# Performance work log

Measured on AMD Instinct MI355X. Metric: run time of the kernel, lower is better.

The kernel has to match this reference:

```python
import jax, jax.numpy as jnp
import numpy as np

T = 256        # number of save/step points
BATCH = 2048   # batched trajectories
DATA = 32      # state dim (data_size)
WIDTH = 128    # MLP width
DELAYS = (1.0, 2.0)  # constant delays tau_j (all >> dt so lookups are in the past)


def setup_inputs() -> dict:
    key = jax.random.key(0)
    ks = jax.random.split(key, 5)
    ts = jnp.linspace(0.0, 10.0, T, dtype=jnp.float32)
    y0 = jax.random.normal(ks[0], (BATCH, DATA), dtype=jnp.float32)
    in_size = (len(DELAYS) + 1) * DATA  # (nb_delays + 1) * data_size

    def lin(k, o, i):
        kw, kb = jax.random.split(k)
        lim = 1.0 / np.sqrt(i)
        W = jax.random.uniform(kw, (o, i), jnp.float32, -lim, lim)
        b = jax.random.uniform(kb, (o,), jnp.float32, -lim, lim)
        return W, b

    W0, b0 = lin(ks[1], WIDTH, in_size)   # in -> width
    W1, b1 = lin(ks[2], WIDTH, WIDTH)     # hidden
    W2, b2 = lin(ks[3], WIDTH, WIDTH)     # hidden
    W3, b3 = lin(ks[4], DATA, WIDTH)      # width -> out (no activation)
    return dict(ts=ts, y0=y0, W0=W0, b0=b0, W1=W1, b1=b1, W2=W2, b2=b2, W3=W3, b3=b3)


def _mlp(x, W0, b0, W1, b1, W2, b2, W3, b3):
    # eqx.nn.MLP(depth=3, activation=relu): 4 linears, relu after hidden layers
    h = jax.nn.relu(x @ W0.T + b0)
    h = jax.nn.relu(h @ W1.T + b1)
    h = jax.nn.relu(h @ W2.T + b2)
    return h @ W3.T + b3


def _solve(ts, y0, params):
    t0 = ts[0]
    dt0 = ts[1] - ts[0]

    def lookup(buf, t):
        # linear interpolation of stored history on the uniform grid;
        # t <= t0 clips to index 0 where buf[0] == y0 (constant initial history)
        s = jnp.clip((t - t0) / dt0, 0.0, T - 1.0)
        i0 = jnp.floor(s).astype(jnp.int32)
        i1 = jnp.minimum(i0 + 1, T - 1)
        w = s - i0.astype(s.dtype)
        return (1.0 - w) * buf[i0] + w * buf[i1]

    def f(t, y, buf):
        hist = [lookup(buf, t - tau) for tau in DELAYS]
        return _mlp(jnp.concatenate([y] + hist, axis=-1), *params)

    buf0 = jnp.zeros((T, BATCH, DATA), y0.dtype).at[0].set(y0)

    def step(carry, inp):
        y, buf = carry
        i, t, t_next = inp
        dt = t_next - t
        # Bosh3 / Bogacki-Shampine stages
        k1 = f(t, y, buf)
        k2 = f(t + 0.5 * dt, y + 0.5 * dt * k1, buf)
        k3 = f(t + 0.75 * dt, y + 0.75 * dt * k2, buf)
        y_next = y + dt * (2.0 / 9.0 * k1 + 1.0 / 3.0 * k2 + 4.0 / 9.0 * k3)
        buf = buf.at[i + 1].set(y_next)
        return (y_next, buf), y_next

    xs = (jnp.arange(T - 1), ts[:-1], ts[1:])
    (_, _), ys_tail = jax.lax.scan(step, (y0, buf0), xs)
    return jnp.concatenate([y0[None], ys_tail], axis=0)  # [T, BATCH, DATA]


def reference(ts, y0, W0, b0, W1, b1, W2, b2, W3, b3):
    ys = _solve(ts, y0, (W0, b0, W1, b1, W2, b2, W3, b3))
    return ys, jnp.int32(T - 1)  # (solution.ys, num_steps)
```

## Files before the change

### kernel.cpp

```cpp
#include <hip/hip_runtime.h>

#define TT 256
#define BATCH 2048
#define DATA 32
#define WSLOTS 52

typedef __bf16 bf16x8 __attribute__((ext_vector_type(8)));
typedef float f32x4 __attribute__((ext_vector_type(4)));

#define MFMA(A, B, C) __builtin_amdgcn_mfma_f32_16x16x32_bf16((A), (B), (C), 0, 0, 0)

union bfp2 { uint2 u; __bf16 b[4]; };
union bfp4 { uint4 q; bf16x8 v; __bf16 b[8]; };

__device__ __forceinline__ bf16x8 ldw8(const float* __restrict__ p) {
    float4 a = *(const float4*)p;
    float4 b = *(const float4*)(p + 4);
    bf16x8 r;
    r[0] = (__bf16)a.x; r[1] = (__bf16)a.y; r[2] = (__bf16)a.z; r[3] = (__bf16)a.w;
    r[4] = (__bf16)b.x; r[5] = (__bf16)b.y; r[6] = (__bf16)b.z; r[7] = (__bf16)b.w;
    return r;
}

__device__ __forceinline__ bf16x8 ldx(const char* base, int row, int kbyte) {
    return *(const bf16x8*)(base + row * 256 + (kbyte ^ ((row & 7) << 4)));
}

#define LERP2(TQT, O1, O2)                                                            \
    {                                                                                 \
        _Pragma("unroll") for (int dl = 0; dl < 2; ++dl) {                            \
            const float tau = dl ? 2.0f : 1.0f;                                       \
            float s = ((TQT) - tau - t0v) * ivd0;                                     \
            s = fminf(fmaxf(s, 0.0f), 255.0f);                                        \
            const int   i0 = (int)s;                                                  \
            const int   i1 = min(i0 + 1, TT - 1);                                     \
            const float w  = s - (float)i0;                                           \
            bfp4 pa, pb, pr;                                                          \
            pa.v = *(const bf16x8*)(hists + (i0 % WSLOTS) * 1280 + m * 80 + g * 16);  \
            pb.v = *(const bf16x8*)(hists + (i1 % WSLOTS) * 1280 + m * 80 + g * 16);  \
            _Pragma("unroll") for (int e = 0; e < 8; ++e) {                           \
                const float va = (float)pa.b[e];                                      \
                pr.b[e] = (__bf16)fmaf(w, (float)pb.b[e] - va, va);                   \
            }                                                                         \
            if (dl == 0) O1 = pr.v; else O2 = pr.v;                                   \
        }                                                                             \
    }

#define SEGB()                                                                        \
    {                                                                                 \
        bf16x8 xf[4];                                                                 \
        _Pragma("unroll") for (int kc = 0; kc < 4; ++kc)                              \
            xf[kc] = ldx(hA, m, kc * 64 + g * 16);                                    \
        f32x4 a0 = b1D, cc = {0.f, 0.f, 0.f, 0.f};                                    \
        __builtin_amdgcn_s_setprio(1);                                                \
        a0 = MFMA(W1f[0], xf[0], a0); cc = MFMA(W1f[2], xf[2], cc);                   \
        a0 = MFMA(W1f[1], xf[1], a0); cc = MFMA(W1f[3], xf[3], cc);                   \
        __builtin_amdgcn_s_setprio(0);                                                \
        bfp2 p0;                                                                      \
        _Pragma("unroll") for (int j = 0; j < 4; ++j)                                 \
            p0.b[j] = (__bf16)fmaxf(a0[j] + cc[j], 0.0f);                             \
        *(uint2*)(hB + m * 256 + ((tbB2 + g * 8) ^ sw)) = p0.u;                       \
    }

#define SEGC(COEF, FIRST, STOREH2, DSTBUF)                                            \
    {                                                                                 \
        bf16x8 xf[4];                                                                 \
        _Pragma("unroll") for (int kc = 0; kc < 4; ++kc)                              \
            xf[kc] = ldx(hB, m, kc * 64 + g * 16);                                    \
        f32x4 a0 = b2D, cc = {0.f, 0.f, 0.f, 0.f};                                    \
        __builtin_amdgcn_s_setprio(1);                                                \
        a0 = MFMA(W2f[0], xf[0], a0); cc = MFMA(W2f[2], xf[2], cc);                   \
        a0 = MFMA(W2f[1], xf[1], a0); cc = MFMA(W2f[3], xf[3], cc);                   \
        __builtin_amdgcn_s_setprio(0);                                                \
        f32x4 r;                                                                      \
        _Pragma("unroll") for (int j = 0; j < 4; ++j)                                 \
            r[j] = fmaxf(a0[j] + cc[j], 0.0f);                                        \
        if (FIRST) { _Pragma("unroll") for (int j = 0; j < 4; ++j)                    \
                         hsreg[j] = (COEF) * r[j]; }                                  \
        else       { _Pragma("unroll") for (int j = 0; j < 4; ++j)                    \
                         hsreg[j] = fmaf((COEF), r[j], hsreg[j]); }                   \
        bfp2 ph;                                                                      \
        if (STOREH2) { _Pragma("unroll") for (int j = 0; j < 4; ++j)                  \
                           ph.b[j] = (__bf16)r[j]; }                                  \
        else         { _Pragma("unroll") for (int j = 0; j < 4; ++j)                  \
                           ph.b[j] = (__bf16)hsreg[j]; }                              \
        *(uint2*)((DSTBUF) + m * 256 + ((tbB2 + g * 8) ^ sw)) = ph.u;                 \
    }

#define SEGA23(HIN, CST)                                                              \
    {                                                                                 \
        bf16x8 hf[4];                                                                 \
        _Pragma("unroll") for (int kc = 0; kc < 4; ++kc)                              \
            hf[kc] = ldx(HIN, m, kc * 64 + g * 16);                                   \
        f32x4 ta = {0.f, 0.f, 0.f, 0.f}, tc = ta;                                     \
        __builtin_amdgcn_s_setprio(1);                                                \
        ta = MFMA(Mf[0], hf[0], ta); tc = MFMA(Mf[2], hf[2], tc);                     \
        ta = MFMA(Mf[1], hf[1], ta); tc = MFMA(Mf[3], hf[3], tc);                     \
        __builtin_amdgcn_s_setprio(0);                                                \
        bf16x8 xl1, xl2;                                                              \
        LERP2(fmaf(CST, dt, t), xl1, xl2)                                             \
        f32x4 la = b0D;                                                               \
        __builtin_amdgcn_s_setprio(1);                                                \
        la = MFMA(W0lf[0], xl1, la);                                                  \
        la = MFMA(W0lf[1], xl2, la);                                                  \
        __builtin_amdgcn_s_setprio(0);                                                \
        const float cdt = (CST) * dt;                                                 \
        bfp2 p0;                                                                      \
        _Pragma("unroll") for (int j = 0; j < 4; ++j)                                 \
            p0.b[j] = (__bf16)fmaxf(fmaf(cdt, ta[j] + tc[j] + c0v[j], u[j]) + la[j],  \
                                    0.0f);                                            \
        *(uint2*)(hA + m * 256 + ((tbB2 + g * 8) ^ sw)) = p0.u;                       \
    }

__global__ __launch_bounds__(512, 1) void dde_fu(
    const float* __restrict__ ts, const float* __restrict__ y0,
    const float* __restrict__ W0, const float* __restrict__ b0,
    const float* __restrict__ W1, const float* __restrict__ b1,
    const float* __restrict__ W2, const float* __restrict__ b2,
    const float* __restrict__ W3, const float* __restrict__ b3,
    float* __restrict__ out)
{
    __shared__ __align__(16) char hists[WSLOTS * 1280];
    __shared__ __align__(16) char hA[16 * 256];
    __shared__ __align__(16) char hB[16 * 256];
    __shared__ __align__(16) char h2a[16 * 256];
    __shared__ __align__(16) char h2b[16 * 256];
    __shared__ __align__(16) char hsb[16 * 256];
    __shared__ __align__(16) float ybuf[512];
    __shared__ float tsb[TT];

    const int tid  = threadIdx.x;
    const int lane = tid & 63;
    const int wv   = tid >> 6;
    const int m    = lane & 15;
    const int g    = lane >> 4;
    const int tbB2 = wv * 32;
    const int sw   = (m & 7) << 4;
    const int R0   = blockIdx.x * 16;

    for (int idx = tid; idx < WSLOTS * 320; idx += 512) ((unsigned*)hists)[idx] = 0u;
    if (tid < TT) tsb[tid] = ts[tid];

    bf16x8 W0lf[2], W1f[4], W2f[4], W3f[4], Mf[4];
    {
        const int rw = wv * 16 + m;
        #pragma unroll
        for (int kc = 0; kc < 2; ++kc) W0lf[kc] = ldw8(W0 + rw * 96 + 32 + kc * 32 + g * 8);
        #pragma unroll
        for (int kc = 0; kc < 4; ++kc) W1f[kc] = ldw8(W1 + rw * 128 + kc * 32 + g * 8);
        #pragma unroll
        for (int kc = 0; kc < 4; ++kc) W2f[kc] = ldw8(W2 + rw * 128 + kc * 32 + g * 8);
        const int rw3 = (wv & 1) * 16 + m;
        #pragma unroll
        for (int kc = 0; kc < 4; ++kc) W3f[kc] = ldw8(W3 + rw3 * 128 + kc * 32 + g * 8);
    }
    {
        float w0y[32];
        const float* w0r = W0 + (wv * 16 + m) * 96;
        #pragma unroll
        for (int d = 0; d < 32; ++d) w0y[d] = w0r[d];
        #pragma unroll
        for (int kc = 0; kc < 4; ++kc) {
            bf16x8 f;
            #pragma unroll
            for (int e = 0; e < 8; ++e) {
                const int h = kc * 32 + g * 8 + e;
                float acc = 0.f;
                #pragma unroll
                for (int d = 0; d < 32; ++d) acc = fmaf(w0y[d], W3[d * 128 + h], acc);
                f[e] = (__bf16)acc;
            }
            Mf[kc] = f;
        }
    }
    f32x4 b0D = *(const f32x4*)(b0 + wv * 16 + g * 4);
    f32x4 b1D = *(const f32x4*)(b1 + wv * 16 + g * 4);
    f32x4 b2D = *(const f32x4*)(b2 + wv * 16 + g * 4);
    f32x4 b3D = *(const f32x4*)(b3 + (wv & 1) * 16 + g * 4);
    f32x4 c0v, u;
    {
        const float* yr = y0 + (R0 + m) * DATA;
        #pragma unroll
        for (int j = 0; j < 4; ++j) {
            const float* w0r = W0 + (wv * 16 + g * 4 + j) * 96;
            float a = 0.f, uu = 0.f;
            #pragma unroll
            for (int d = 0; d < 32; ++d) {
                a  = fmaf(w0r[d], b3[d], a);
                uu = fmaf(w0r[d], yr[d], uu);
            }
            c0v[j] = a; u[j] = uu;
        }
    }
    f32x4 y;
    #pragma unroll
    for (int j = 0; j < 4; ++j)
        y[j] = y0[(R0 + m) * DATA + (wv & 1) * 16 + g * 4 + j];

    __syncthreads();

    if (wv == 0) {
        float4 v0 = *(const float4*)(y0 + (R0 + m) * DATA + g * 8);
        float4 v1 = *(const float4*)(y0 + (R0 + m) * DATA + g * 8 + 4);
        bfp4 p;
        p.b[0] = (__bf16)v0.x; p.b[1] = (__bf16)v0.y;
        p.b[2] = (__bf16)v0.z; p.b[3] = (__bf16)v0.w;
        p.b[4] = (__bf16)v1.x; p.b[5] = (__bf16)v1.y;
        p.b[6] = (__bf16)v1.z; p.b[7] = (__bf16)v1.w;
        *(bf16x8*)(hists + m * 80 + g * 16) = p.v;
        *(float4*)(out + (R0 + m) * DATA + g * 8) = v0;
        *(float4*)(out + (R0 + m) * DATA + g * 8 + 4) = v1;
    }
    if (blockIdx.x == 0 && tid == 0)
        out[(size_t)TT * BATCH * DATA] = 255.0f;
    __syncthreads();

    const float t0v  = tsb[0];
    const float ivd0 = 1.0f / (tsb[1] - tsb[0]);

    #pragma unroll 1
    for (int i = 0; i < TT - 1; ++i) {
        const float t  = tsb[i];
        const float dt = tsb[i + 1] - t;
        f32x4 hsreg;

        {
            if (i > 0) {
                const float dtp = t - tsb[i - 1];
                bf16x8 hs[4];
                #pragma unroll
                for (int kc = 0; kc < 4; ++kc) hs[kc] = ldx(hsb, m, kc * 64 + g * 16);
                f32x4 ta = {0.f, 0.f, 0.f, 0.f}, tc = ta;
                __builtin_amdgcn_s_setprio(1);
                ta = MFMA(Mf[0], hs[0], ta); tc = MFMA(Mf[2], hs[2], tc);
                ta = MFMA(Mf[1], hs[1], ta); tc = MFMA(Mf[3], hs[3], tc);
                __builtin_amdgcn_s_setprio(0);
                #pragma unroll
                for (int j = 0; j < 4; ++j)
                    u[j] = fmaf(dtp, ta[j] + tc[j] + c0v[j], u[j]);
                if (wv < 2) {
                    f32x4 ya = {0.f, 0.f, 0.f, 0.f}, yc = ya;
                    __builtin_amdgcn_s_setprio(1);
                    ya = MFMA(W3f[0], hs[0], ya); yc = MFMA(W3f[2], hs[2], yc);
                    ya = MFMA(W3f[1], hs[1], ya); yc = MFMA(W3f[3], hs[3], yc);
                    __builtin_amdgcn_s_setprio(0);
                    #pragma unroll
                    for (int j = 0; j < 4; ++j) {
                        y[j] = fmaf(dtp, ya[j] + yc[j] + b3D[j], y[j]);
                        *(__bf16*)(hists + (i % WSLOTS) * 1280 + m * 80
                                   + wv * 32 + g * 8 + 2 * j) = (__bf16)y[j];
                        ybuf[m * 32 + wv * 16 + g * 4 + j] = y[j];
                    }
                }
            }
            bf16x8 xl1, xl2;
            LERP2(t, xl1, xl2)
            f32x4 la = b0D;
            __builtin_amdgcn_s_setprio(1);
            la = MFMA(W0lf[0], xl1, la);
            la = MFMA(W0lf[1], xl2, la);
            __builtin_amdgcn_s_setprio(0);
            bfp2 p0;
            #pragma unroll
            for (int j = 0; j < 4; ++j)
                p0.b[j] = (__bf16)fmaxf(u[j] + la[j], 0.0f);
            *(uint2*)(hA + m * 256 + ((tbB2 + g * 8) ^ sw)) = p0.u;
        }
        __syncthreads();
        SEGB()
        __syncthreads();
        SEGC(2.0f / 9.0f, 1, 1, h2a)
        if (i > 0 && wv < 2) {
            const int L = wv * 64 + lane;
            float4 yv = *(const float4*)(ybuf + L * 4);
            *(float4*)(out + (size_t)i * BATCH * DATA
                       + (R0 + (L >> 3)) * DATA + (L & 7) * 4) = yv;
        }
        __syncthreads();
        SEGA23(h2a, 0.5f)
        __syncthreads();
        SEGB()
        __syncthreads();
        SEGC(1.0f / 3.0f, 0, 1, h2b)
        __syncthreads();
        SEGA23(h2b, 0.75f)
        __syncthreads();
        SEGB()
        __syncthreads();
        SEGC(4.0f / 9.0f, 0, 0, hsb)
        __syncthreads();
    }

    if (wv < 2) {
        const float dtp = tsb[TT - 1] - tsb[TT - 2];
        bf16x8 hs[4];
        #pragma unroll
        for (int kc = 0; kc < 4; ++kc) hs[kc] = ldx(hsb, m, kc * 64 + g * 16);
        f32x4 ya = {0.f, 0.f, 0.f, 0.f}, yc = ya;
        ya = MFMA(W3f[0], hs[0], ya); yc = MFMA(W3f[2], hs[2], yc);
        ya = MFMA(W3f[1], hs[1], ya); yc = MFMA(W3f[3], hs[3], yc);
        #pragma unroll
        for (int j = 0; j < 4; ++j) {
            y[j] = fmaf(dtp, ya[j] + yc[j] + b3D[j], y[j]);
            ybuf[m * 32 + (wv & 1) * 16 + g * 4 + j] = y[j];
        }
    }
    __syncthreads();
    if (wv < 2) {
        const int L = wv * 64 + lane;
        float4 yv = *(const float4*)(ybuf + L * 4);
        *(float4*)(out + (size_t)(TT - 1) * BATCH * DATA
                   + (R0 + (L >> 3)) * DATA + (L & 7) * 4) = yv;
    }
}

extern "C" void kernel_launch(void* const* d_in, const int* in_sizes, int n_in,
                              void* d_out, int out_size, void* d_ws, size_t ws_size,
                              hipStream_t stream) {
    const float* ts = (const float*)d_in[0];
    const float* y0 = (const float*)d_in[1];
    const float* W0 = (const float*)d_in[2];
    const float* b0 = (const float*)d_in[3];
    const float* W1 = (const float*)d_in[4];
    const float* b1 = (const float*)d_in[5];
    const float* W2 = (const float*)d_in[6];
    const float* b2 = (const float*)d_in[7];
    const float* W3 = (const float*)d_in[8];
    const float* b3 = (const float*)d_in[9];

    dde_fu<<<dim3(BATCH / 16), dim3(512), 0, stream>>>(
        ts, y0, W0, b0, W1, b1, W2, b2, W3, b3, (float*)d_out);
}
```

Baseline: 842.0 us.

## Prefetch delayed-history interpolation into the previous stage and build the fused matrix with MFMA

```diff
diff --git a/kernel.cpp b/kernel.cpp
--- a/kernel.cpp
+++ b/kernel.cpp
@@ -46,7 +46,7 @@
         }                                                                             \
     }
 
-#define SEGB()                                                                        \
+#define SEGB_PF(TQ2, O1, O2)                                                          \
     {                                                                                 \
         bf16x8 xf[4];                                                                 \
         _Pragma("unroll") for (int kc = 0; kc < 4; ++kc)                              \
@@ -56,6 +56,7 @@
         a0 = MFMA(W1f[0], xf[0], a0); cc = MFMA(W1f[2], xf[2], cc);                   \
         a0 = MFMA(W1f[1], xf[1], a0); cc = MFMA(W1f[3], xf[3], cc);                   \
         __builtin_amdgcn_s_setprio(0);                                                \
+        LERP2(TQ2, O1, O2)                                                            \
         bfp2 p0;                                                                      \
         _Pragma("unroll") for (int j = 0; j < 4; ++j)                                 \
             p0.b[j] = (__bf16)fmaxf(a0[j] + cc[j], 0.0f);                             \
@@ -87,22 +88,18 @@
         *(uint2*)((DSTBUF) + m * 256 + ((tbB2 + g * 8) ^ sw)) = ph.u;                 \
     }
 
-#define SEGA23(HIN, CST)                                                              \
+#define SEGA_F(HIN, CST, XL1, XL2)                                                    \
     {                                                                                 \
         bf16x8 hf[4];                                                                 \
         _Pragma("unroll") for (int kc = 0; kc < 4; ++kc)                              \
             hf[kc] = ldx(HIN, m, kc * 64 + g * 16);                                   \
+        f32x4 la = b0D;                                                               \
         f32x4 ta = {0.f, 0.f, 0.f, 0.f}, tc = ta;                                     \
         __builtin_amdgcn_s_setprio(1);                                                \
+        la = MFMA(W0lf[0], XL1, la);                 \
+        la = MFMA(W0lf[1], XL2, la);                                                  \
         ta = MFMA(Mf[0], hf[0], ta); tc = MFMA(Mf[2], hf[2], tc);                     \
         ta = MFMA(Mf[1], hf[1], ta); tc = MFMA(Mf[3], hf[3], tc);                     \
-        __builtin_amdgcn_s_setprio(0);                                                \
-        bf16x8 xl1, xl2;                                                              \
-        LERP2(fmaf(CST, dt, t), xl1, xl2)                                             \
-        f32x4 la = b0D;                                                               \
-        __builtin_amdgcn_s_setprio(1);                                                \
-        la = MFMA(W0lf[0], xl1, la);                                                  \
-        la = MFMA(W0lf[1], xl2, la);                                                  \
         __builtin_amdgcn_s_setprio(0);                                                \
         const float cdt = (CST) * dt;                                                 \
         bfp2 p0;                                                                      \
@@ -112,7 +109,7 @@
         *(uint2*)(hA + m * 256 + ((tbB2 + g * 8) ^ sw)) = p0.u;                       \
     }
 
-__global__ __launch_bounds__(512, 1) void dde_fu(
+__global__ __launch_bounds__(512, 1) void dde_f2(
     const float* __restrict__ ts, const float* __restrict__ y0,
     const float* __restrict__ W0, const float* __restrict__ b0,
     const float* __restrict__ W1, const float* __restrict__ b1,
@@ -121,6 +118,7 @@
     float* __restrict__ out)
 {
     __shared__ __align__(16) char hists[WSLOTS * 1280];
+    __shared__ __align__(16) char Mlds[128 * 256];
     __shared__ __align__(16) char hA[16 * 256];
     __shared__ __align__(16) char hB[16 * 256];
     __shared__ __align__(16) char h2a[16 * 256];
@@ -141,7 +139,7 @@
     for (int idx = tid; idx < WSLOTS * 320; idx += 512) ((unsigned*)hists)[idx] = 0u;
     if (tid < TT) tsb[tid] = ts[tid];
 
-    bf16x8 W0lf[2], W1f[4], W2f[4], W3f[4], Mf[4];
+    bf16x8 W0lf[2], W1f[4], W2f[4], W3f[4];
     {
         const int rw = wv * 16 + m;
         #pragma unroll
@@ -155,22 +153,21 @@
         for (int kc = 0; kc < 4; ++kc) W3f[kc] = ldw8(W3 + rw3 * 128 + kc * 32 + g * 8);
     }
     {
-        float w0y[32];
-        const float* w0r = W0 + (wv * 16 + m) * 96;
-        #pragma unroll
-        for (int d = 0; d < 32; ++d) w0y[d] = w0r[d];
-        #pragma unroll
-        for (int kc = 0; kc < 4; ++kc) {
-            bf16x8 f;
+        bf16x8 Af = ldw8(W0 + (wv * 16 + m) * 96 + g * 8);
+        #pragma unroll
+        for (int ht = 0; ht < 8; ++ht) {
+            bf16x8 Bf;
             #pragma unroll
-            for (int e = 0; e < 8; ++e) {
-                const int h = kc * 32 + g * 8 + e;
-                float acc = 0.f;
-                #pragma unroll
-                for (int d = 0; d < 32; ++d) acc = fmaf(w0y[d], W3[d * 128 + h], acc);
-                f[e] = (__bf16)acc;
+            for (int e = 0; e < 8; ++e)
+                Bf[e] = (__bf16)W3[(g * 8 + e) * 128 + ht * 16 + m];
+            f32x4 d = {0.f, 0.f, 0.f, 0.f};
+            d = MFMA(Af, Bf, d);
+            #pragma unroll
+            for (int j = 0; j < 4; ++j) {
+                const int r = wv * 16 + g * 4 + j;
+                *(__bf16*)(Mlds + r * 256 + (((ht * 16 + m) * 2) ^ ((r & 7) << 4)))
+                    = (__bf16)d[j];
             }
-            Mf[kc] = f;
         }
     }
     f32x4 b0D = *(const f32x4*)(b0 + wv * 16 + g * 4);
@@ -198,6 +195,10 @@
         y[j] = y0[(R0 + m) * DATA + (wv & 1) * 16 + g * 4 + j];
 
     __syncthreads();
+
+    bf16x8 Mf[4];
+    #pragma unroll
+    for (int kc = 0; kc < 4; ++kc) Mf[kc] = ldx(Mlds, wv * 16 + m, kc * 64 + g * 16);
 
     if (wv == 0) {
         float4 v0 = *(const float4*)(y0 + (R0 + m) * DATA + g * 8);
@@ -218,10 +219,14 @@
     const float t0v  = tsb[0];
     const float ivd0 = 1.0f / (tsb[1] - tsb[0]);
 
+    bf16x8 xl1a, xl1b, xl2a, xl2b, xl3a, xl3b;
+    LERP2(t0v, xl1a, xl1b)
+
     #pragma unroll 1
     for (int i = 0; i < TT - 1; ++i) {
         const float t  = tsb[i];
-        const float dt = tsb[i + 1] - t;
+        const float tn = tsb[i + 1];
+        const float dt = tn - t;
         f32x4 hsreg;
 
         {
@@ -253,12 +258,10 @@
                     }
                 }
             }
-            bf16x8 xl1, xl2;
-            LERP2(t, xl1, xl2)
             f32x4 la = b0D;
             __builtin_amdgcn_s_setprio(1);
-            la = MFMA(W0lf[0], xl1, la);
-            la = MFMA(W0lf[1], xl2, la);
+            la = MFMA(W0lf[0], xl1a, la);
+            la = MFMA(W0lf[1], xl1b, la);
             __builtin_amdgcn_s_setprio(0);
             bfp2 p0;
             #pragma unroll
@@ -267,7 +270,7 @@
             *(uint2*)(hA + m * 256 + ((tbB2 + g * 8) ^ sw)) = p0.u;
         }
         __syncthreads();
-        SEGB()
+        SEGB_PF(fmaf(0.5f, dt, t), xl2a, xl2b)
         __syncthreads();
         SEGC(2.0f / 9.0f, 1, 1, h2a)
         if (i > 0 && wv < 2) {
@@ -277,15 +280,15 @@
                        + (R0 + (L >> 3)) * DATA + (L & 7) * 4) = yv;
         }
         __syncthreads();
-        SEGA23(h2a, 0.5f)
-        __syncthreads();
-        SEGB()
+        SEGA_F(h2a, 0.5f, xl2a, xl2b)
+        __syncthreads();
+        SEGB_PF(fmaf(0.75f, dt, t), xl3a, xl3b)
         __syncthreads();
         SEGC(1.0f / 3.0f, 0, 1, h2b)
         __syncthreads();
-        SEGA23(h2b, 0.75f)
-        __syncthreads();
-        SEGB()
+        SEGA_F(h2b, 0.75f, xl3a, xl3b)
+        __syncthreads();
+        SEGB_PF(tn, xl1a, xl1b)
         __syncthreads();
         SEGC(4.0f / 9.0f, 0, 0, hsb)
         __syncthreads();
@@ -328,6 +331,6 @@
     const float* W3 = (const float*)d_in[8];
     const float* b3 = (const float*)d_in[9];
 
-    dde_fu<<<dim3(BATCH / 16), dim3(512), 0, stream>>>(
+    dde_f2<<<dim3(BATCH / 16), dim3(512), 0, stream>>>(
         ts, y0, W0, b0, W1, b1, W2, b2, W3, b3, (float*)d_out);
 }
```

Measured after the change: 824.2 us. 1.02x faster.
